# Performance work log

Measured on AMD Instinct MI355X. Metric: run time of the kernel, lower is better.

The kernel has to match this reference:

```python
import jax, jax.numpy as jnp
import numpy as np
import math

B, S, D, H = 4, 2048, 1024, 16
HD = D // H  # head_dim = 64


def setup_inputs() -> dict:
    key = jax.random.key(0)
    ks = jax.random.split(key, 7)
    s = 0.02
    return {
        "q": jax.random.normal(ks[0], (B, S, D), jnp.float32),
        "k": jax.random.normal(ks[1], (B, S, D), jnp.float32),
        "v": jax.random.normal(ks[2], (B, S, D), jnp.float32),
        "wq": jax.random.normal(ks[3], (D, D), jnp.float32) * s,
        "wk": jax.random.normal(ks[4], (D, D), jnp.float32) * s,
        "wv": jax.random.normal(ks[5], (D, D), jnp.float32) * s,
        "wo": jax.random.normal(ks[6], (D, D), jnp.float32) * s,
    }


def reference(q, k, v, wq, wk, wv, wo):
    # Linear (no bias): y = x @ W.T, W is (out, in)
    xq = jnp.einsum('bsd,ed->bse', q, wq).reshape(B, S, H, HD).transpose(0, 2, 1, 3)
    xk = jnp.einsum('bsd,ed->bse', k, wk).reshape(B, S, H, HD).transpose(0, 2, 1, 3)
    xv = jnp.einsum('bsd,ed->bse', v, wv).reshape(B, S, H, HD).transpose(0, 2, 1, 3)
    scores = jnp.einsum('bhqd,bhkd->bhqk', xq, xk) / math.sqrt(HD)  # [B,H,S,S]
    causal = jnp.tril(jnp.ones((S, S), dtype=bool))
    scores = jnp.where(causal[None, None], scores, jnp.float32(-jnp.inf))
    probs = jax.nn.softmax(scores, axis=-1)  # dropout p=0 -> identity
    out = jnp.einsum('bhqk,bhkd->bhqd', probs, xv)  # [B,H,S,HD]
    out = out.transpose(0, 2, 1, 3).reshape(B, S, D)
    return jnp.einsum('bsd,ed->bse', out, wo)
```

## Files before the change

kernel.cpp:

```cpp
#include <hip/hip_runtime.h>

#define SS 2048
#define DD 1024
#define HH 16
#define HD 64
#define MM 8192

typedef unsigned short ushort_t;
typedef __attribute__((ext_vector_type(8))) short short8;
typedef __attribute__((ext_vector_type(4))) float f32x4;
typedef __attribute__((ext_vector_type(4))) unsigned short us4;
typedef __attribute__((ext_vector_type(8))) unsigned short us8;

__device__ __forceinline__ ushort_t f2bf(float f) {
    union { float f; unsigned u; } x; x.f = f;
    unsigned r = x.u + 0x7fffu + ((x.u >> 16) & 1u);
    return (ushort_t)(r >> 16);
}
__device__ __forceinline__ float bf2f(ushort_t h) {
    union { unsigned u; float f; } x; x.u = ((unsigned)h) << 16; return x.f;
}
__device__ __forceinline__ unsigned pack_bf2(float a, float b) {
    union { float f; unsigned u; } x, y; x.f = a; y.f = b;
    return __builtin_amdgcn_perm(y.u, x.u, 0x07060302u);
}

__device__ __forceinline__ void async16(const void* g, void* l) {
    __builtin_amdgcn_global_load_lds(
        (const __attribute__((address_space(1))) unsigned int*)g,
        (__attribute__((address_space(3))) unsigned int*)l, 16, 0, 0);
}

__global__ void cvt_all(const float* __restrict__ q, const float* __restrict__ k,
                        const float* __restrict__ v, const float* __restrict__ wq,
                        const float* __restrict__ wk, const float* __restrict__ wv,
                        const float* __restrict__ wo, ushort_t* __restrict__ qbf,
                        ushort_t* __restrict__ kbf, ushort_t* __restrict__ vbf,
                        ushort_t* __restrict__ wbf) {
    long i = ((long)blockIdx.x * 256 + threadIdx.x) * 8;
    const float* src; ushort_t* dst;
    if (i < (3l << 23)) {
        int s = (int)(i >> 23);
        long off = i & ((1l << 23) - 1);
        src = ((s == 0) ? q : (s == 1) ? k : v) + off;
        dst = ((s == 0) ? qbf : (s == 1) ? kbf : vbf) + off;
    } else {
        long j = i - (3l << 23);
        int s = (int)(j >> 20);
        src = ((s == 0) ? wq : (s == 1) ? wk : (s == 2) ? wv : wo) + (j & 1048575);
        dst = wbf + j;
    }
    float4 f0 = *(const float4*)src;
    float4 f1 = *(const float4*)(src + 4);
    us8 o;
    o[0] = f2bf(f0.x); o[1] = f2bf(f0.y); o[2] = f2bf(f0.z); o[3] = f2bf(f0.w);
    o[4] = f2bf(f1.x); o[5] = f2bf(f1.y); o[6] = f2bf(f1.z); o[7] = f2bf(f1.w);
    *(us8*)dst = o;
}

__device__ __forceinline__ void epi_store(int row, int col, float vf, int mode,
                                          void* Yv) {
    if (mode == 2) {
        ((float*)Yv)[(size_t)row * DD + col] = vf;
    } else {
        ushort_t vh = f2bf(vf);
        int b = row >> 11, s = row & 2047;
        int h = col >> 6,  hd = col & 63;
        if (mode == 0) {
            ((ushort_t*)Yv)[(((size_t)b * HH + h) * SS + s) * HD + hd] = vh;
        } else {
            int sp = (s & ~63) | (((s & 15) << 2) | ((s >> 4) & 3));
            ((ushort_t*)Yv)[(((size_t)b * HH + h) * HD + hd) * SS + sp] = vh;
        }
    }
}

__device__ __forceinline__ void gemm128_body(const ushort_t* __restrict__ A,
                                             const ushort_t* __restrict__ Bw,
                                             int m0, int n0, int mode, void* Y,
                                             ushort_t (*As)[128 * 32],
                                             ushort_t (*Bs)[128 * 32]) {
    int tid = threadIdx.x;
    int w = tid >> 6, lane = tid & 63;
    int l16 = lane & 15, quad = lane >> 4;
    int wm = (w >> 2) * 64, wn = (w & 3) * 32;

    f32x4 acc[4][2];
    #pragma unroll
    for (int i = 0; i < 4; ++i)
        #pragma unroll
        for (int j = 0; j < 2; ++j) acc[i][j] = (f32x4){0.f, 0.f, 0.f, 0.f};

    int r0 = tid >> 2, j0 = ((tid & 3) ^ (r0 & 3)) * 8;
    int swA = (quad ^ (l16 & 3)) * 8;

    const ushort_t* Ar0 = A  + (size_t)(m0 + r0) * DD + j0;
    const ushort_t* Br0 = Bw + (size_t)(n0 + r0) * DD + j0;
    int ldsb = w * 64 * 8;

    async16(Ar0,      &As[0][ldsb]);
    async16(Br0,      &Bs[0][ldsb]);
    async16(Ar0 + 32, &As[1][ldsb]);
    async16(Br0 + 32, &Bs[1][ldsb]);

    int c = 0, c2 = 2;
    for (int kk = 0; kk < 32; ++kk) {
        __builtin_amdgcn_s_barrier();
        if (kk < 30) {
            int k2 = (kk + 2) * 32;
            async16(Ar0 + k2, &As[c2][ldsb]);
            async16(Br0 + k2, &Bs[c2][ldsb]);
            asm volatile("s_waitcnt vmcnt(4)" ::: "memory");
        } else if (kk == 30) {
            asm volatile("s_waitcnt vmcnt(2)" ::: "memory");
        } else {
            asm volatile("s_waitcnt vmcnt(0)" ::: "memory");
        }
        __builtin_amdgcn_s_barrier();
        __builtin_amdgcn_sched_barrier(0);

        short8 af[4], bfr[2];
        #pragma unroll
        for (int t = 0; t < 4; ++t)
            af[t] = *(const short8*)&As[c][(wm + t * 16 + l16) * 32 + swA];
        #pragma unroll
        for (int t = 0; t < 2; ++t)
            bfr[t] = *(const short8*)&Bs[c][(wn + t * 16 + l16) * 32 + swA];
        #pragma unroll
        for (int mt = 0; mt < 4; ++mt)
            #pragma unroll
            for (int nt = 0; nt < 2; ++nt)
                acc[mt][nt] = __builtin_amdgcn_mfma_f32_16x16x32_bf16(af[mt], bfr[nt], acc[mt][nt], 0, 0, 0);

        c  = (c  == 2) ? 0 : c  + 1;
        c2 = (c2 == 2) ? 0 : c2 + 1;
    }

    #pragma unroll
    for (int mt = 0; mt < 4; ++mt)
        #pragma unroll
        for (int r = 0; r < 4; ++r) {
            int row = m0 + wm + mt * 16 + quad * 4 + r;
            #pragma unroll
            for (int nt = 0; nt < 2; ++nt)
                epi_store(row, n0 + wn + nt * 16 + l16, acc[mt][nt][r], mode, Y);
        }
}

__global__ __launch_bounds__(512) void proj3f(const ushort_t* __restrict__ qbf,
                                              const ushort_t* __restrict__ kbf,
                                              const ushort_t* __restrict__ vbf,
                                              const ushort_t* __restrict__ Wall,
                                              ushort_t* __restrict__ xq,
                                              ushort_t* __restrict__ xk,
                                              ushort_t* __restrict__ xvT) {
    __shared__ __align__(16) ushort_t As[3][128 * 32];
    __shared__ __align__(16) ushort_t Bs[3][128 * 32];
    int mat   = (int)(blockIdx.x >> 9);
    int inner = (int)(blockIdx.x & 511);
    int m0 = (inner & 63) * 128;
    int n0 = (inner >> 6) * 128;
    const ushort_t* A  = (mat == 0) ? qbf : (mat == 1) ? kbf : vbf;
    const ushort_t* Bw = Wall + ((size_t)mat << 20);
    void* Y = (mat == 0) ? (void*)xq : (mat == 1) ? (void*)xk : (void*)xvT;
    gemm128_body(A, Bw, m0, n0, (mat == 2) ? 1 : 0, Y, As, Bs);
}

__global__ __launch_bounds__(512) void out_gemm(const ushort_t* __restrict__ Abf,
                                                const ushort_t* __restrict__ Bw,
                                                float* __restrict__ Y) {
    __shared__ __align__(16) ushort_t As[3][128 * 32];
    __shared__ __align__(16) ushort_t Bs[3][128 * 32];
    int m0 = (int)(blockIdx.x & 63) * 128;
    int n0 = (int)(blockIdx.x >> 6) * 128;
    gemm128_body(Abf, Bw, m0, n0, 2, (void*)Y, As, Bs);
}

__global__ __launch_bounds__(512) void attn_kernel(const ushort_t* __restrict__ xq,
                                                   const ushort_t* __restrict__ xk,
                                                   const ushort_t* __restrict__ xvT,
                                                   ushort_t* __restrict__ ao) {
    __shared__ __align__(16) ushort_t Ksm[2][64 * 64];
    __shared__ __align__(16) ushort_t Vsm[2][64 * 64];
    __shared__ __align__(16) ushort_t Psm[8][16 * 72];

    int tid = threadIdx.x;
    int w = tid >> 6, lane = tid & 63;
    int l16 = lane & 15, quad = lane >> 4;
    int bh = blockIdx.x & 63;
    int p  = blockIdx.x >> 6;
    int b = bh >> 4, h = bh & 15;

    const ushort_t* Q  = xq  + (size_t)bh * SS * HD;
    const ushort_t* K  = xk  + (size_t)bh * SS * HD;
    const ushort_t* VT = xvT + (size_t)bh * HD * SS;

    int r0 = tid >> 3, j0 = ((tid & 7) ^ (r0 & 7)) * 8;
    int ldsb = (w * 64) * 8;

    short8 ones;
    #pragma unroll
    for (int i = 0; i < 8; ++i) ones[i] = (short)0x3F80;

    const float CS = 0.125f * 1.44269504f;

    for (int ph = 0; ph < 2; ++ph) {
        int qt = ph ? (15 - p) : p;
        int qb = qt * 128;
        int qmin = qb + w * 16;
        int ktmax = 2 * qt + 1;

        short8 aq[2];
        #pragma unroll
        for (int kc = 0; kc < 2; ++kc) {
            short8 t = *(const short8*)(Q + (size_t)(qmin + l16) * HD + kc * 32 + quad * 8);
            #pragma unroll
            for (int i = 0; i < 8; ++i)
                t[i] = (short)f2bf(bf2f((ushort_t)t[i]) * CS);
            aq[kc] = t;
        }

        f32x4 o[4];
        #pragma unroll
        for (int dt = 0; dt < 4; ++dt) o[dt] = (f32x4){0.f, 0.f, 0.f, 0.f};
        f32x4 lacc = (f32x4){0.f, 0.f, 0.f, 0.f};

        __syncthreads();
        async16(K  + (size_t)r0 * HD + j0, &Ksm[0][ldsb]);
        async16(VT + (size_t)r0 * SS + j0, &Vsm[0][ldsb]);

        for (int kt = 0; kt <= ktmax; ++kt) {
            int kb = kt * 64;
            int c = kt & 1;
            __syncthreads();
            if (kt < ktmax) {
                int kb1 = kb + 64;
                async16(K  + (size_t)(kb1 + r0) * HD + j0, &Ksm[c ^ 1][ldsb]);
                async16(VT + (size_t)r0 * SS + kb1 + j0, &Vsm[c ^ 1][ldsb]);
            }

            f32x4 sc[4];
            __builtin_amdgcn_s_setprio(1);
            #pragma unroll
            for (int nt = 0; nt < 4; ++nt) {
                int row = nt * 16 + l16;
                short8 bk0 = *(const short8*)&Ksm[c][row * 64 + ((0 + quad) ^ (l16 & 7)) * 8];
                short8 bk1 = *(const short8*)&Ksm[c][row * 64 + ((4 + quad) ^ (l16 & 7)) * 8];
                f32x4 cc = (f32x4){0.f, 0.f, 0.f, 0.f};
                cc = __builtin_amdgcn_mfma_f32_16x16x32_bf16(aq[0], bk0, cc, 0, 0, 0);
                cc = __builtin_amdgcn_mfma_f32_16x16x32_bf16(aq[1], bk1, cc, 0, 0, 0);
                sc[nt] = cc;
            }
            __builtin_amdgcn_s_setprio(0);

            bool msk = (kb + 63 > qmin);
            #pragma unroll
            for (int r = 0; r < 4; ++r) {
                float e0, e1, e2, e3;
                if (msk) {
                    int qg = qmin + quad * 4 + r;
                    e0 = (kb +  0 + l16 <= qg) ? __builtin_amdgcn_exp2f(sc[0][r]) : 0.f;
                    e1 = (kb + 16 + l16 <= qg) ? __builtin_amdgcn_exp2f(sc[1][r]) : 0.f;
                    e2 = (kb + 32 + l16 <= qg) ? __builtin_amdgcn_exp2f(sc[2][r]) : 0.f;
                    e3 = (kb + 48 + l16 <= qg) ? __builtin_amdgcn_exp2f(sc[3][r]) : 0.f;
                } else {
                    e0 = __builtin_amdgcn_exp2f(sc[0][r]);
                    e1 = __builtin_amdgcn_exp2f(sc[1][r]);
                    e2 = __builtin_amdgcn_exp2f(sc[2][r]);
                    e3 = __builtin_amdgcn_exp2f(sc[3][r]);
                }
                uint2 pk = { pack_bf2(e0, e1), pack_bf2(e2, e3) };
                *(uint2*)&Psm[w][(quad * 4 + r) * 72 + l16 * 4] = pk;
            }

            asm volatile("s_waitcnt lgkmcnt(0)" ::: "memory");

            __builtin_amdgcn_s_setprio(1);
            #pragma unroll
            for (int kc = 0; kc < 2; ++kc) {
                short8 ap = *(const short8*)&Psm[w][l16 * 72 + kc * 32 + quad * 8];
                lacc = __builtin_amdgcn_mfma_f32_16x16x32_bf16(ap, ones, lacc, 0, 0, 0);
                #pragma unroll
                for (int dt = 0; dt < 4; ++dt) {
                    int row = dt * 16 + l16;
                    short8 bv = *(const short8*)&Vsm[c][row * 64 + ((kc * 4 + quad) ^ (l16 & 7)) * 8];
                    o[dt] = __builtin_amdgcn_mfma_f32_16x16x32_bf16(ap, bv, o[dt], 0, 0, 0);
                }
            }
            __builtin_amdgcn_s_setprio(0);
        }

        #pragma unroll
        for (int r = 0; r < 4; ++r) {
            float inv = 1.0f / lacc[r];
            int qg = qmin + quad * 4 + r;
            #pragma unroll
            for (int dt = 0; dt < 4; ++dt)
                ao[((size_t)(b * SS + qg)) * DD + h * HD + dt * 16 + l16] = f2bf(o[dt][r] * inv);
        }
    }
}

extern "C" void kernel_launch(void* const* d_in, const int* in_sizes, int n_in,
                              void* d_out, int out_size, void* d_ws, size_t ws_size,
                              hipStream_t stream) {
    const float* q  = (const float*)d_in[0];
    const float* k  = (const float*)d_in[1];
    const float* v  = (const float*)d_in[2];
    const float* wq = (const float*)d_in[3];
    const float* wk = (const float*)d_in[4];
    const float* wv = (const float*)d_in[5];
    const float* wo = (const float*)d_in[6];
    float* out = (float*)d_out;

    ushort_t* wbf = (ushort_t*)d_ws;
    ushort_t* xq  = wbf + 4194304ull;
    ushort_t* xk  = xq  + 8388608ull;
    ushort_t* xvT = xk  + 8388608ull;
    ushort_t* ao  = xvT + 8388608ull;
    ushort_t* vbf = ao;
    ushort_t* qbf = (ushort_t*)d_out;
    ushort_t* kbf = qbf + 8388608ull;

    cvt_all<<<14336, 256, 0, stream>>>(q, k, v, wq, wk, wv, wo, qbf, kbf, vbf, wbf);
    proj3f<<<1536, 512, 0, stream>>>(qbf, kbf, vbf, wbf, xq, xk, xvT);
    attn_kernel<<<512, 512, 0, stream>>>(xq, xk, xvT, ao);
    out_gemm<<<512, 512, 0, stream>>>(ao, wbf + 3145728ull, out);
}
```

Before: 313.1 us.

## Fuse paired causal query tiles into one KV sweep sharing K/V loads

```diff
diff --git a/kernel.cpp b/kernel.cpp
--- a/kernel.cpp
+++ b/kernel.cpp
@@ -176,6 +176,63 @@
     gemm128_body(Abf, Bw, m0, n0, 2, (void*)Y, As, Bs);
 }
 
+__device__ __forceinline__ void attn_tile(int kb, int qmin, const short8 aq[2],
+                                          const ushort_t* __restrict__ Ks,
+                                          const ushort_t* __restrict__ Vs,
+                                          ushort_t* __restrict__ Pw,
+                                          f32x4 o[4], f32x4& lacc, short8 ones,
+                                          int l16, int quad) {
+    f32x4 sc[4];
+    __builtin_amdgcn_s_setprio(1);
+    #pragma unroll
+    for (int nt = 0; nt < 4; ++nt) {
+        int row = nt * 16 + l16;
+        short8 bk0 = *(const short8*)&Ks[row * 64 + ((0 + quad) ^ (l16 & 7)) * 8];
+        short8 bk1 = *(const short8*)&Ks[row * 64 + ((4 + quad) ^ (l16 & 7)) * 8];
+        f32x4 cc = (f32x4){0.f, 0.f, 0.f, 0.f};
+        cc = __builtin_amdgcn_mfma_f32_16x16x32_bf16(aq[0], bk0, cc, 0, 0, 0);
+        cc = __builtin_amdgcn_mfma_f32_16x16x32_bf16(aq[1], bk1, cc, 0, 0, 0);
+        sc[nt] = cc;
+    }
+    __builtin_amdgcn_s_setprio(0);
+
+    bool msk = (kb + 63 > qmin);
+    #pragma unroll
+    for (int r = 0; r < 4; ++r) {
+        float e0, e1, e2, e3;
+        if (msk) {
+            int qg = qmin + quad * 4 + r;
+            e0 = (kb +  0 + l16 <= qg) ? __builtin_amdgcn_exp2f(sc[0][r]) : 0.f;
+            e1 = (kb + 16 + l16 <= qg) ? __builtin_amdgcn_exp2f(sc[1][r]) : 0.f;
+            e2 = (kb + 32 + l16 <= qg) ? __builtin_amdgcn_exp2f(sc[2][r]) : 0.f;
+            e3 = (kb + 48 + l16 <= qg) ? __builtin_amdgcn_exp2f(sc[3][r]) : 0.f;
+        } else {
+            e0 = __builtin_amdgcn_exp2f(sc[0][r]);
+            e1 = __builtin_amdgcn_exp2f(sc[1][r]);
+            e2 = __builtin_amdgcn_exp2f(sc[2][r]);
+            e3 = __builtin_amdgcn_exp2f(sc[3][r]);
+        }
+        uint2 pk = { pack_bf2(e0, e1), pack_bf2(e2, e3) };
+        *(uint2*)&Pw[(quad * 4 + r) * 72 + l16 * 4] = pk;
+    }
+
+    asm volatile("s_waitcnt lgkmcnt(0)" ::: "memory");
+
+    __builtin_amdgcn_s_setprio(1);
+    #pragma unroll
+    for (int kc = 0; kc < 2; ++kc) {
+        short8 ap = *(const short8*)&Pw[l16 * 72 + kc * 32 + quad * 8];
+        lacc = __builtin_amdgcn_mfma_f32_16x16x32_bf16(ap, ones, lacc, 0, 0, 0);
+        #pragma unroll
+        for (int dt = 0; dt < 4; ++dt) {
+            int row = dt * 16 + l16;
+            short8 bv = *(const short8*)&Vs[row * 64 + ((kc * 4 + quad) ^ (l16 & 7)) * 8];
+            o[dt] = __builtin_amdgcn_mfma_f32_16x16x32_bf16(ap, bv, o[dt], 0, 0, 0);
+        }
+    }
+    __builtin_amdgcn_s_setprio(0);
+}
+
 __global__ __launch_bounds__(512) void attn_kernel(const ushort_t* __restrict__ xq,
                                                    const ushort_t* __restrict__ xk,
                                                    const ushort_t* __restrict__ xvT,
@@ -204,99 +261,63 @@
 
     const float CS = 0.125f * 1.44269504f;
 
-    for (int ph = 0; ph < 2; ++ph) {
-        int qt = ph ? (15 - p) : p;
-        int qb = qt * 128;
-        int qmin = qb + w * 16;
-        int ktmax = 2 * qt + 1;
-
-        short8 aq[2];
-        #pragma unroll
-        for (int kc = 0; kc < 2; ++kc) {
-            short8 t = *(const short8*)(Q + (size_t)(qmin + l16) * HD + kc * 32 + quad * 8);
-            #pragma unroll
-            for (int i = 0; i < 8; ++i)
-                t[i] = (short)f2bf(bf2f((ushort_t)t[i]) * CS);
-            aq[kc] = t;
-        }
-
-        f32x4 o[4];
-        #pragma unroll
-        for (int dt = 0; dt < 4; ++dt) o[dt] = (f32x4){0.f, 0.f, 0.f, 0.f};
-        f32x4 lacc = (f32x4){0.f, 0.f, 0.f, 0.f};
-
+    int qmin_lo = p * 128 + w * 16;
+    int qmin_hi = (15 - p) * 128 + w * 16;
+    int ktmax   = 2 * (15 - p) + 1;
+
+    short8 aqlo[2], aqhi[2];
+    #pragma unroll
+    for (int kc = 0; kc < 2; ++kc) {
+        short8 t0 = *(const short8*)(Q + (size_t)(qmin_lo + l16) * HD + kc * 32 + quad * 8);
+        short8 t1 = *(const short8*)(Q + (size_t)(qmin_hi + l16) * HD + kc * 32 + quad * 8);
+        #pragma unroll
+        for (int i = 0; i < 8; ++i) {
+            t0[i] = (short)f2bf(bf2f((ushort_t)t0[i]) * CS);
+            t1[i] = (short)f2bf(bf2f((ushort_t)t1[i]) * CS);
+        }
+        aqlo[kc] = t0; aqhi[kc] = t1;
+    }
+
+    f32x4 olo[4], ohi[4];
+    #pragma unroll
+    for (int dt = 0; dt < 4; ++dt) {
+        olo[dt] = (f32x4){0.f, 0.f, 0.f, 0.f};
+        ohi[dt] = (f32x4){0.f, 0.f, 0.f, 0.f};
+    }
+    f32x4 lacclo = (f32x4){0.f, 0.f, 0.f, 0.f};
+    f32x4 lacchi = (f32x4){0.f, 0.f, 0.f, 0.f};
+
+    async16(K  + (size_t)r0 * HD + j0, &Ksm[0][ldsb]);
+    async16(VT + (size_t)r0 * SS + j0, &Vsm[0][ldsb]);
+
+    for (int kt = 0; kt <= ktmax; ++kt) {
+        int kb = kt * 64;
+        int c = kt & 1;
         __syncthreads();
-        async16(K  + (size_t)r0 * HD + j0, &Ksm[0][ldsb]);
-        async16(VT + (size_t)r0 * SS + j0, &Vsm[0][ldsb]);
-
-        for (int kt = 0; kt <= ktmax; ++kt) {
-            int kb = kt * 64;
-            int c = kt & 1;
-            __syncthreads();
-            if (kt < ktmax) {
-                int kb1 = kb + 64;
-                async16(K  + (size_t)(kb1 + r0) * HD + j0, &Ksm[c ^ 1][ldsb]);
-                async16(VT + (size_t)r0 * SS + kb1 + j0, &Vsm[c ^ 1][ldsb]);
-            }
-
-            f32x4 sc[4];
-            __builtin_amdgcn_s_setprio(1);
-            #pragma unroll
-            for (int nt = 0; nt < 4; ++nt) {
-                int row = nt * 16 + l16;
-                short8 bk0 = *(const short8*)&Ksm[c][row * 64 + ((0 + quad) ^ (l16 & 7)) * 8];
-                short8 bk1 = *(const short8*)&Ksm[c][row * 64 + ((4 + quad) ^ (l16 & 7)) * 8];
-                f32x4 cc = (f32x4){0.f, 0.f, 0.f, 0.f};
-                cc = __builtin_amdgcn_mfma_f32_16x16x32_bf16(aq[0], bk0, cc, 0, 0, 0);
-                cc = __builtin_amdgcn_mfma_f32_16x16x32_bf16(aq[1], bk1, cc, 0, 0, 0);
-                sc[nt] = cc;
-            }
-            __builtin_amdgcn_s_setprio(0);
-
-            bool msk = (kb + 63 > qmin);
-            #pragma unroll
-            for (int r = 0; r < 4; ++r) {
-                float e0, e1, e2, e3;
-                if (msk) {
-                    int qg = qmin + quad * 4 + r;
-                    e0 = (kb +  0 + l16 <= qg) ? __builtin_amdgcn_exp2f(sc[0][r]) : 0.f;
-                    e1 = (kb + 16 + l16 <= qg) ? __builtin_amdgcn_exp2f(sc[1][r]) : 0.f;
-                    e2 = (kb + 32 + l16 <= qg) ? __builtin_amdgcn_exp2f(sc[2][r]) : 0.f;
-                    e3 = (kb + 48 + l16 <= qg) ? __builtin_amdgcn_exp2f(sc[3][r]) : 0.f;
-                } else {
-                    e0 = __builtin_amdgcn_exp2f(sc[0][r]);
-                    e1 = __builtin_amdgcn_exp2f(sc[1][r]);
-                    e2 = __builtin_amdgcn_exp2f(sc[2][r]);
-                    e3 = __builtin_amdgcn_exp2f(sc[3][r]);
-                }
-                uint2 pk = { pack_bf2(e0, e1), pack_bf2(e2, e3) };
-                *(uint2*)&Psm[w][(quad * 4 + r) * 72 + l16 * 4] = pk;
-            }
-
-            asm volatile("s_waitcnt lgkmcnt(0)" ::: "memory");
-
-            __builtin_amdgcn_s_setprio(1);
-            #pragma unroll
-            for (int kc = 0; kc < 2; ++kc) {
-                short8 ap = *(const short8*)&Psm[w][l16 * 72 + kc * 32 + quad * 8];
-                lacc = __builtin_amdgcn_mfma_f32_16x16x32_bf16(ap, ones, lacc, 0, 0, 0);
-                #pragma unroll
-                for (int dt = 0; dt < 4; ++dt) {
-                    int row = dt * 16 + l16;
-                    short8 bv = *(const short8*)&Vsm[c][row * 64 + ((kc * 4 + quad) ^ (l16 & 7)) * 8];
-                    o[dt] = __builtin_amdgcn_mfma_f32_16x16x32_bf16(ap, bv, o[dt], 0, 0, 0);
-                }
-            }
-            __builtin_amdgcn_s_setprio(0);
-        }
-
-        #pragma unroll
-        for (int r = 0; r < 4; ++r) {
-            float inv = 1.0f / lacc[r];
-            int qg = qmin + quad * 4 + r;
-            #pragma unroll
-            for (int dt = 0; dt < 4; ++dt)
-                ao[((size_t)(b * SS + qg)) * DD + h * HD + dt * 16 + l16] = f2bf(o[dt][r] * inv);
+        if (kt < ktmax) {
+            int kb1 = kb + 64;
+            async16(K  + (size_t)(kb1 + r0) * HD + j0, &Ksm[c ^ 1][ldsb]);
+            async16(VT + (size_t)r0 * SS + kb1 + j0, &Vsm[c ^ 1][ldsb]);
+        }
+
+        if (kb <= qmin_lo + 15)
+            attn_tile(kb, qmin_lo, aqlo, &Ksm[c][0], &Vsm[c][0], &Psm[w][0],
+                      olo, lacclo, ones, l16, quad);
+        if (kb <= qmin_hi + 15)
+            attn_tile(kb, qmin_hi, aqhi, &Ksm[c][0], &Vsm[c][0], &Psm[w][0],
+                      ohi, lacchi, ones, l16, quad);
+    }
+
+    #pragma unroll
+    for (int r = 0; r < 4; ++r) {
+        float invl = 1.0f / lacclo[r];
+        float invh = 1.0f / lacchi[r];
+        int qgl = qmin_lo + quad * 4 + r;
+        int qgh = qmin_hi + quad * 4 + r;
+        #pragma unroll
+        for (int dt = 0; dt < 4; ++dt) {
+            ao[((size_t)(b * SS + qgl)) * DD + h * HD + dt * 16 + l16] = f2bf(olo[dt][r] * invl);
+            ao[((size_t)(b * SS + qgh)) * DD + h * HD + dt * 16 + l16] = f2bf(ohi[dt][r] * invh);
         }
     }
 }
```

Result: no change. 307.7 us (median of 4 runs) (-1.7%).
